# Kernel optimization log

Hardware: AMD Instinct MI355X
Metric: run time of the kernel (lower is better)

The kernel has to match this reference:

```python
import jax, jax.numpy as jnp
import numpy as np

B, L, D, H, FF, NB = 131072, 9, 22, 2, 128, 19


def setup_inputs() -> dict:
    key = jax.random.key(0)
    ks = jax.random.split(key, 20)
    def p(k, shape):
        return jax.random.normal(k, shape, dtype=jnp.float32) * 0.05
    return dict(
        seq_embd=jax.random.normal(ks[0], (B, L, D), dtype=jnp.float32),
        W_rel=p(ks[1], (NB, D)), b_rel=p(ks[2], (D,)),
        Wq=p(ks[3], (D, D * H)), Wk=p(ks[4], (D, D * H)), Wv=p(ks[5], (D, D * H)),
        Wo=p(ks[6], (D * H, D)),
        g_att=jnp.ones((D,), jnp.float32), b_att=jnp.zeros((D,), jnp.float32),
        W1=p(ks[7], (D, FF)), b1=p(ks[8], (FF,)),
        W2=p(ks[9], (FF, D)), b2=p(ks[10], (D,)),
        Wp=p(ks[11], (D, H)), bp=p(ks[12], (H,)),
        g_ff=jnp.ones((D,), jnp.float32), b_ff=jnp.zeros((D,), jnp.float32),
        W_res=p(ks[13], (D, 1)), b_res=p(ks[14], (1,)),
        W_out=p(ks[15], (L, 2)), b_out=p(ks[16], (2,)),
    )


def _layernorm(x, g, b, eps=1e-5):
    m = x.mean(-1, keepdims=True)
    v = ((x - m) ** 2).mean(-1, keepdims=True)
    return (x - m) / jnp.sqrt(v + eps) * g + b


def reference(seq_embd, W_rel, b_rel, Wq, Wk, Wv, Wo, g_att, b_att,
              W1, b1, W2, b2, Wp, bp, g_ff, b_ff, W_res, b_res, W_out, b_out):
    # --- absolute sinusoidal positional encoding (d_model=22, max_len=9) ---
    pos = jnp.arange(L, dtype=jnp.float32)[:, None]
    div = jnp.exp(jnp.arange(0, D, 2, dtype=jnp.float32) * (-jnp.log(10000.0) / D))
    pe = jnp.zeros((L, D), jnp.float32)
    pe = pe.at[:, 0::2].set(jnp.sin(pos * div)).at[:, 1::2].set(jnp.cos(pos * div))
    x = seq_embd + pe  # [B, L, D]

    # --- relative position encoding (identical for every batch row) ---
    ri = jnp.arange(L, dtype=jnp.float32)
    diff = ri[:, None] - ri[None, :]                     # [L, L]
    bounds = jnp.arange(-9, 10, dtype=jnp.float32)       # 19 bins
    idx = jnp.argmin(jnp.abs(diff[..., None] - bounds), axis=-1)
    rel = jax.nn.one_hot(idx, NB, dtype=jnp.float32) @ W_rel + b_rel  # [L, L, D]

    # attention bias: pos_enc_linear then permute to [H, L, L]
    pbias = jnp.transpose(rel @ Wp + bp, (2, 0, 1))       # [H, L, L]

    # --- self-attention ---
    q = (x @ Wq).reshape(-1, L, H, D).transpose(0, 2, 1, 3)  # [B,H,L,D]
    k = (x @ Wk).reshape(-1, L, H, D).transpose(0, 2, 1, 3)
    v = (x @ Wv).reshape(-1, L, H, D).transpose(0, 2, 1, 3)
    a = jnp.einsum('bhid,bhjd->bhij', q, k) / jnp.sqrt(jnp.float32(D)) + pbias
    a = jax.nn.softmax(a, axis=-1)
    heads = jnp.einsum('bhij,bhjd->bhid', a, v)
    heads = heads.transpose(0, 2, 1, 3).reshape(-1, L, H * D)
    y = heads @ Wo
    x = _layernorm(x + y, g_att, b_att)

    # --- feed-forward ---
    y = jax.nn.relu(x @ W1 + b1) @ W2 + b2
    x = _layernorm(x + y, g_ff, b_ff)

    # --- heads: residue linear then output linear over sequence dim ---
    p_res = (x @ W_res + b_res)[..., 0]  # [B, L]
    return p_res @ W_out + b_out         # [B, 2]
```

## Files before the change

kernel.cpp:

```cpp
#include <hip/hip_runtime.h>

#define B_TOT 131072
#define L_ 9
#define D_ 22
#define H_ 2
#define FF_ 128
#define RPB 28
#define TPB (RPB * L_)

#define WS_PE   0
#define WS_PB   198
#define WS_MT   360
#define WS_VWO  1328
#define WS_W1T  2296

__global__ void setup_k(const float* __restrict__ W_rel, const float* __restrict__ b_rel,
                        const float* __restrict__ Wq, const float* __restrict__ Wk,
                        const float* __restrict__ Wv, const float* __restrict__ Wo,
                        const float* __restrict__ W1, const float* __restrict__ Wp,
                        const float* __restrict__ bp, float* __restrict__ ws)
{
    const int t = threadIdx.x;
    for (int idx = t; idx < 198; idx += 256) {
        int l = idx / 22, d = idx % 22, tt = d / 2;
        float div = __expf((float)(2 * tt) * (-logf(10000.f) / 22.f));
        float ang = (float)l * div;
        ws[WS_PE + idx] = (d & 1) ? cosf(ang) : sinf(ang);
    }
    for (int idx = t; idx < 162; idx += 256) {
        int h = idx / 81, rem = idx % 81, i = rem / 9, j = rem % 9;
        float s = bp[h];
        for (int d = 0; d < 22; ++d)
            s += (W_rel[(i - j + 9) * 22 + d] + b_rel[d]) * Wp[d * 2 + h];
        ws[WS_PB + idx] = s;
    }
    for (int idx = t; idx < 968; idx += 256) {
        int h = idx / 484, rem = idx % 484, cp = rem / 22, c = rem % 22;
        float s = 0.f;
        for (int e = 0; e < 22; ++e)
            s += Wq[c * 44 + h * 22 + e] * Wk[cp * 44 + h * 22 + e];
        ws[WS_MT + idx] = s * 0.21320071635561041f;
    }
    for (int idx = t; idx < 968; idx += 256) {
        int h = idx / 484, rem = idx % 484, d = rem / 22, c = rem % 22;
        float s = 0.f;
        for (int e = 0; e < 22; ++e)
            s += Wv[c * 44 + h * 22 + e] * Wo[(h * 22 + e) * 22 + d];
        ws[WS_VWO + idx] = s;
    }
    for (int idx = t; idx < 2816; idx += 256) {
        int f = idx / 22, c = idx % 22;
        ws[WS_W1T + idx] = W1[c * 128 + f];
    }
}

__global__ __launch_bounds__(TPB) void fused_model(
    const float* __restrict__ seq, const float* __restrict__ ws,
    const float* __restrict__ g_att, const float* __restrict__ b_att,
    const float* __restrict__ b1, const float* __restrict__ W2,
    const float* __restrict__ b2, const float* __restrict__ g_ff,
    const float* __restrict__ b_ff, const float* __restrict__ W_res,
    const float* __restrict__ b_res, const float* __restrict__ W_out,
    const float* __restrict__ b_out, float* __restrict__ out)
{
    __shared__ __align__(16) float xbuf[RPB][L_][24];
    __shared__ __align__(16) float vwbuf[RPB][L_][24];
    __shared__ float red[RPB][L_][2];

    const int tid = threadIdx.x;
    const int r = tid / L_;
    const int i = tid - r * L_;
    const long g = (long)blockIdx.x * RPB + r;
    const bool active = g < B_TOT;
    const long gc = active ? g : (long)(B_TOT - 1);

    float x[D_];
    {
        const float* xin = seq + gc * (L_ * D_) + i * D_;
        const float* pe  = ws + WS_PE + i * D_;
        #pragma unroll
        for (int c = 0; c < D_; c += 2) {
            float2 t = *reinterpret_cast<const float2*>(xin + c);
            x[c]     = t.x + pe[c];
            x[c + 1] = t.y + pe[c + 1];
        }
    }
    #pragma unroll
    for (int c = 0; c < D_; ++c) xbuf[r][i][c] = x[c];

    float att[D_];
    #pragma unroll
    for (int c = 0; c < D_; ++c) att[c] = 0.f;

    for (int h = 0; h < H_; ++h) {
        const float* MT   = ws + WS_MT  + h * (D_ * D_);
        const float* WVOT = ws + WS_VWO + h * (D_ * D_);
        const float* pb   = ws + WS_PB  + h * (L_ * L_) + i * L_;

        #pragma unroll 2
        for (int d = 0; d < D_; ++d) {
            float s = 0.f;
            #pragma unroll
            for (int c = 0; c < D_; ++c) s += x[c] * WVOT[d * D_ + c];
            vwbuf[r][i][d] = s;
        }
        __syncthreads();

        float qm[D_];
        #pragma unroll
        for (int d = 0; d < D_; ++d) {
            float s = 0.f;
            #pragma unroll
            for (int c = 0; c < D_; ++c) s += x[c] * MT[d * D_ + c];
            qm[d] = s;
        }

        float p[L_];
        float mx = -1e30f;
        #pragma unroll
        for (int j = 0; j < L_; ++j) {
            float s = pb[j];
            #pragma unroll
            for (int c = 0; c < D_; ++c) s += qm[c] * xbuf[r][j][c];
            p[j] = s;
            mx = fmaxf(mx, s);
        }
        float sum = 0.f;
        #pragma unroll
        for (int j = 0; j < L_; ++j) { p[j] = __expf(p[j] - mx); sum += p[j]; }
        const float inv = 1.f / sum;

        #pragma unroll
        for (int j = 0; j < L_; ++j) {
            const float pj = p[j] * inv;
            #pragma unroll
            for (int c = 0; c < D_; ++c) att[c] += pj * vwbuf[r][j][c];
        }
        __syncthreads();
    }

    {
        float s = 0.f;
        #pragma unroll
        for (int c = 0; c < D_; ++c) { x[c] += att[c]; s += x[c]; }
        const float mean = s * (1.f / 22.f);
        float vs = 0.f;
        #pragma unroll
        for (int c = 0; c < D_; ++c) { float d = x[c] - mean; vs += d * d; }
        const float rstd = rsqrtf(vs * (1.f / 22.f) + 1e-5f);
        #pragma unroll
        for (int c = 0; c < D_; ++c) x[c] = (x[c] - mean) * rstd * g_att[c] + b_att[c];
    }

    float y2[D_];
    #pragma unroll
    for (int c = 0; c < D_; ++c) y2[c] = b2[c];
    {
        const float* W1T = ws + WS_W1T;
        #pragma unroll 4
        for (int f = 0; f < FF_; ++f) {
            float s = b1[f];
            #pragma unroll
            for (int c = 0; c < D_; ++c) s += x[c] * W1T[f * D_ + c];
            s = fmaxf(s, 0.f);
            #pragma unroll
            for (int c = 0; c < D_; ++c) y2[c] += s * W2[f * D_ + c];
        }
    }

    {
        float s = 0.f;
        #pragma unroll
        for (int c = 0; c < D_; ++c) { x[c] += y2[c]; s += x[c]; }
        const float mean = s * (1.f / 22.f);
        float vs = 0.f;
        #pragma unroll
        for (int c = 0; c < D_; ++c) { float d = x[c] - mean; vs += d * d; }
        const float rstd = rsqrtf(vs * (1.f / 22.f) + 1e-5f);
        #pragma unroll
        for (int c = 0; c < D_; ++c) x[c] = (x[c] - mean) * rstd * g_ff[c] + b_ff[c];
    }

    {
        float pr = b_res[0];
        #pragma unroll
        for (int c = 0; c < D_; ++c) pr += x[c] * W_res[c];
        red[r][i][0] = pr * W_out[i * 2 + 0];
        red[r][i][1] = pr * W_out[i * 2 + 1];
    }
    __syncthreads();
    if (i == 0 && active) {
        float o0 = b_out[0], o1 = b_out[1];
        #pragma unroll
        for (int j = 0; j < L_; ++j) { o0 += red[r][j][0]; o1 += red[r][j][1]; }
        float2 o; o.x = o0; o.y = o1;
        *reinterpret_cast<float2*>(out + g * 2) = o;
    }
}

extern "C" void kernel_launch(void* const* d_in, const int* in_sizes, int n_in,
                              void* d_out, int out_size, void* d_ws, size_t ws_size,
                              hipStream_t stream)
{
    const float* seq   = (const float*)d_in[0];
    const float* W_rel = (const float*)d_in[1];
    const float* b_rel = (const float*)d_in[2];
    const float* Wq    = (const float*)d_in[3];
    const float* Wk    = (const float*)d_in[4];
    const float* Wv    = (const float*)d_in[5];
    const float* Wo    = (const float*)d_in[6];
    const float* g_att = (const float*)d_in[7];
    const float* b_att = (const float*)d_in[8];
    const float* W1    = (const float*)d_in[9];
    const float* b1    = (const float*)d_in[10];
    const float* W2    = (const float*)d_in[11];
    const float* b2    = (const float*)d_in[12];
    const float* Wp    = (const float*)d_in[13];
    const float* bp    = (const float*)d_in[14];
    const float* g_ff  = (const float*)d_in[15];
    const float* b_ff  = (const float*)d_in[16];
    const float* W_res = (const float*)d_in[17];
    const float* b_res = (const float*)d_in[18];
    const float* W_out = (const float*)d_in[19];
    const float* b_out = (const float*)d_in[20];
    float* out = (float*)d_out;
    float* ws  = (float*)d_ws;

    setup_k<<<1, 256, 0, stream>>>(W_rel, b_rel, Wq, Wk, Wv, Wo, W1, Wp, bp, ws);

    const int grid = (B_TOT + RPB - 1) / RPB;
    fused_model<<<grid, TPB, 0, stream>>>(seq, ws, g_att, b_att, b1, W2, b2,
                                          g_ff, b_ff, W_res, b_res, W_out, b_out, out);
}
```

Measured before the change: 484.9 us.

## Reuse one shared buffer for x, V and reduction; batch both heads' scores

Drops the separate vwbuf and red shared arrays and reuses xbuf for the positional input, then each head's value projection, then the final reduction. Both heads' attention scores are computed first against the shared x rows, and the bias is preloaded into registers. Shared-memory accesses become float4 loads and stores, and launch bounds now request a minimum of 5 blocks to raise occupancy. The cost is extra __syncthreads per head and register pressure from holding both score vectors, which the launch-bound cap could push into spills.

```diff
diff --git a/kernel.cpp b/kernel.cpp
--- a/kernel.cpp
+++ b/kernel.cpp
@@ -54,7 +54,7 @@
     }
 }
 
-__global__ __launch_bounds__(TPB) void fused_model(
+__global__ __launch_bounds__(TPB, 5) void fused_model(
     const float* __restrict__ seq, const float* __restrict__ ws,
     const float* __restrict__ g_att, const float* __restrict__ b_att,
     const float* __restrict__ b1, const float* __restrict__ W2,
@@ -64,8 +64,6 @@
     const float* __restrict__ b_out, float* __restrict__ out)
 {
     __shared__ __align__(16) float xbuf[RPB][L_][24];
-    __shared__ __align__(16) float vwbuf[RPB][L_][24];
-    __shared__ float red[RPB][L_][2];
 
     const int tid = threadIdx.x;
     const int r = tid / L_;
@@ -74,6 +72,15 @@
     const bool active = g < B_TOT;
     const long gc = active ? g : (long)(B_TOT - 1);
 
+    float p0[L_], p1[L_];
+    {
+        const float* pb = ws + WS_PB + i * L_;
+        #pragma unroll
+        for (int j = 0; j < L_; ++j) p0[j] = pb[j];
+        #pragma unroll
+        for (int j = 0; j < L_; ++j) p1[j] = pb[81 + j];
+    }
+
     float x[D_];
     {
         const float* xin = seq + gc * (L_ * D_) + i * D_;
@@ -85,58 +92,108 @@
             x[c + 1] = t.y + pe[c + 1];
         }
     }
-    #pragma unroll
-    for (int c = 0; c < D_; ++c) xbuf[r][i][c] = x[c];
-
-    float att[D_];
-    #pragma unroll
-    for (int c = 0; c < D_; ++c) att[c] = 0.f;
-
+    {
+        float4* row = reinterpret_cast<float4*>(&xbuf[r][i][0]);
+        row[0] = make_float4(x[0], x[1], x[2], x[3]);
+        row[1] = make_float4(x[4], x[5], x[6], x[7]);
+        row[2] = make_float4(x[8], x[9], x[10], x[11]);
+        row[3] = make_float4(x[12], x[13], x[14], x[15]);
+        row[4] = make_float4(x[16], x[17], x[18], x[19]);
+        row[5] = make_float4(x[20], x[21], 0.f, 0.f);
+    }
+    __syncthreads();
+
+    #pragma unroll
     for (int h = 0; h < H_; ++h) {
-        const float* MT   = ws + WS_MT  + h * (D_ * D_);
-        const float* WVOT = ws + WS_VWO + h * (D_ * D_);
-        const float* pb   = ws + WS_PB  + h * (L_ * L_) + i * L_;
-
-        #pragma unroll 2
+        const float* MT = ws + WS_MT + h * (D_ * D_);
+        float qm[D_];
+        #pragma unroll
         for (int d = 0; d < D_; ++d) {
             float s = 0.f;
             #pragma unroll
-            for (int c = 0; c < D_; ++c) s += x[c] * WVOT[d * D_ + c];
-            vwbuf[r][i][d] = s;
-        }
-        __syncthreads();
-
-        float qm[D_];
-        #pragma unroll
-        for (int d = 0; d < D_; ++d) {
-            float s = 0.f;
-            #pragma unroll
             for (int c = 0; c < D_; ++c) s += x[c] * MT[d * D_ + c];
             qm[d] = s;
         }
-
-        float p[L_];
+        float* p = h ? p1 : p0;
+        #pragma unroll
+        for (int j = 0; j < L_; ++j) {
+            const float4* xr = reinterpret_cast<const float4*>(&xbuf[r][j][0]);
+            float4 a0 = xr[0], a1 = xr[1], a2 = xr[2], a3 = xr[3], a4 = xr[4];
+            float2 a5 = *reinterpret_cast<const float2*>(&xbuf[r][j][20]);
+            float s = p[j];
+            s += qm[0]*a0.x + qm[1]*a0.y + qm[2]*a0.z + qm[3]*a0.w;
+            s += qm[4]*a1.x + qm[5]*a1.y + qm[6]*a1.z + qm[7]*a1.w;
+            s += qm[8]*a2.x + qm[9]*a2.y + qm[10]*a2.z + qm[11]*a2.w;
+            s += qm[12]*a3.x + qm[13]*a3.y + qm[14]*a3.z + qm[15]*a3.w;
+            s += qm[16]*a4.x + qm[17]*a4.y + qm[18]*a4.z + qm[19]*a4.w;
+            s += qm[20]*a5.x + qm[21]*a5.y;
+            p[j] = s;
+        }
+    }
+
+    {
         float mx = -1e30f;
         #pragma unroll
+        for (int j = 0; j < L_; ++j) mx = fmaxf(mx, p0[j]);
+        float sum = 0.f;
+        #pragma unroll
+        for (int j = 0; j < L_; ++j) { p0[j] = __expf(p0[j] - mx); sum += p0[j]; }
+        const float inv = 1.f / sum;
+        #pragma unroll
+        for (int j = 0; j < L_; ++j) p0[j] *= inv;
+    }
+    {
+        float mx = -1e30f;
+        #pragma unroll
+        for (int j = 0; j < L_; ++j) mx = fmaxf(mx, p1[j]);
+        float sum = 0.f;
+        #pragma unroll
+        for (int j = 0; j < L_; ++j) { p1[j] = __expf(p1[j] - mx); sum += p1[j]; }
+        const float inv = 1.f / sum;
+        #pragma unroll
+        for (int j = 0; j < L_; ++j) p1[j] *= inv;
+    }
+
+    float att[D_];
+    #pragma unroll
+    for (int c = 0; c < D_; ++c) att[c] = 0.f;
+
+    #pragma unroll
+    for (int h = 0; h < H_; ++h) {
+        const float* WVOT = ws + WS_VWO + h * (D_ * D_);
+        const float* p = h ? p1 : p0;
+        __syncthreads();
+        {
+            float vt[D_];
+            #pragma unroll
+            for (int d = 0; d < D_; ++d) {
+                float s = 0.f;
+                #pragma unroll
+                for (int c = 0; c < D_; ++c) s += x[c] * WVOT[d * D_ + c];
+                vt[d] = s;
+            }
+            float4* row = reinterpret_cast<float4*>(&xbuf[r][i][0]);
+            row[0] = make_float4(vt[0], vt[1], vt[2], vt[3]);
+            row[1] = make_float4(vt[4], vt[5], vt[6], vt[7]);
+            row[2] = make_float4(vt[8], vt[9], vt[10], vt[11]);
+            row[3] = make_float4(vt[12], vt[13], vt[14], vt[15]);
+            row[4] = make_float4(vt[16], vt[17], vt[18], vt[19]);
+            row[5] = make_float4(vt[20], vt[21], 0.f, 0.f);
+        }
+        __syncthreads();
+        #pragma unroll
         for (int j = 0; j < L_; ++j) {
-            float s = pb[j];
-            #pragma unroll
-            for (int c = 0; c < D_; ++c) s += qm[c] * xbuf[r][j][c];
-            p[j] = s;
-            mx = fmaxf(mx, s);
-        }
-        float sum = 0.f;
-        #pragma unroll
-        for (int j = 0; j < L_; ++j) { p[j] = __expf(p[j] - mx); sum += p[j]; }
-        const float inv = 1.f / sum;
-
-        #pragma unroll
-        for (int j = 0; j < L_; ++j) {
-            const float pj = p[j] * inv;
-            #pragma unroll
-            for (int c = 0; c < D_; ++c) att[c] += pj * vwbuf[r][j][c];
-        }
-        __syncthreads();
+            const float4* xr = reinterpret_cast<const float4*>(&xbuf[r][j][0]);
+            float4 a0 = xr[0], a1 = xr[1], a2 = xr[2], a3 = xr[3], a4 = xr[4];
+            float2 a5 = *reinterpret_cast<const float2*>(&xbuf[r][j][20]);
+            const float pj = p[j];
+            att[0]  += pj * a0.x; att[1]  += pj * a0.y; att[2]  += pj * a0.z; att[3]  += pj * a0.w;
+            att[4]  += pj * a1.x; att[5]  += pj * a1.y; att[6]  += pj * a1.z; att[7]  += pj * a1.w;
+            att[8]  += pj * a2.x; att[9]  += pj * a2.y; att[10] += pj * a2.z; att[11] += pj * a2.w;
+            att[12] += pj * a3.x; att[13] += pj * a3.y; att[14] += pj * a3.z; att[15] += pj * a3.w;
+            att[16] += pj * a4.x; att[17] += pj * a4.y; att[18] += pj * a4.z; att[19] += pj * a4.w;
+            att[20] += pj * a5.x; att[21] += pj * a5.y;
+        }
     }
 
     {
@@ -181,18 +238,21 @@
         for (int c = 0; c < D_; ++c) x[c] = (x[c] - mean) * rstd * g_ff[c] + b_ff[c];
     }
 
-    {
-        float pr = b_res[0];
-        #pragma unroll
-        for (int c = 0; c < D_; ++c) pr += x[c] * W_res[c];
-        red[r][i][0] = pr * W_out[i * 2 + 0];
-        red[r][i][1] = pr * W_out[i * 2 + 1];
-    }
+    float* red = reinterpret_cast<float*>(xbuf);
+    float pr = b_res[0];
+    #pragma unroll
+    for (int c = 0; c < D_; ++c) pr += x[c] * W_res[c];
+    __syncthreads();
+    red[tid * 2 + 0] = pr * W_out[i * 2 + 0];
+    red[tid * 2 + 1] = pr * W_out[i * 2 + 1];
     __syncthreads();
     if (i == 0 && active) {
         float o0 = b_out[0], o1 = b_out[1];
         #pragma unroll
-        for (int j = 0; j < L_; ++j) { o0 += red[r][j][0]; o1 += red[r][j][1]; }
+        for (int j = 0; j < L_; ++j) {
+            o0 += red[(r * L_ + j) * 2 + 0];
+            o1 += red[(r * L_ + j) * 2 + 1];
+        }
         float2 o; o.x = o0; o.y = o1;
         *reinterpret_cast<float2*>(out + g * 2) = o;
     }
```

After: 663.1 us. +36.7%, slower.
